# Optimization experiments

Hardware: AMD Instinct MI355X
Metric: run time of the kernel (lower is better)

Reference implementation:

```python
import jax, jax.numpy as jnp
import numpy as np

N_NODES = 100000
N_EDGES = 1600000
IN_DIM, HID_DIM, OUT_DIM = 128, 128, 64


def _sage_conv(x, src, dst, W_l, W_r, b, num_nodes):
    # messages: gather source-node features, mean-aggregate at destination
    msgs = x[src]                                            # [E, D]
    agg = jax.ops.segment_sum(msgs, dst, num_segments=num_nodes)   # [N, D]
    deg = jax.ops.segment_sum(jnp.ones((src.shape[0],), x.dtype), dst,
                              num_segments=num_nodes)        # [N]
    mean = jnp.where(deg[:, None] > 0, agg / jnp.maximum(deg, 1.0)[:, None], 0.0)
    # PyG SAGEConv: lin_l(aggr) + lin_r(root); bias lives in lin_l
    return mean @ W_l + b + x @ W_r


def setup_inputs() -> dict:
    key = jax.random.key(0)
    ks = jax.random.split(key, 8)
    x = jax.random.normal(ks[0], (N_NODES, IN_DIM), dtype=jnp.float32)
    edge_index = jax.random.randint(ks[1], (2, N_EDGES), 0, N_NODES, dtype=jnp.int64)
    s1 = 1.0 / np.sqrt(IN_DIM)
    s2 = 1.0 / np.sqrt(HID_DIM)
    return {
        "x": x,
        "edge_index": edge_index,
        "W1_l": jax.random.normal(ks[2], (IN_DIM, HID_DIM), jnp.float32) * s1,
        "W1_r": jax.random.normal(ks[3], (IN_DIM, HID_DIM), jnp.float32) * s1,
        "b1": jnp.zeros((HID_DIM,), jnp.float32),
        "W2_l": jax.random.normal(ks[4], (HID_DIM, OUT_DIM), jnp.float32) * s2,
        "W2_r": jax.random.normal(ks[5], (HID_DIM, OUT_DIM), jnp.float32) * s2,
        "b2": jnp.zeros((OUT_DIM,), jnp.float32),
    }


def reference(x, edge_index, W1_l, W1_r, b1, W2_l, W2_r, b2):
    src, dst = edge_index[0], edge_index[1]  # source_to_target flow
    h = _sage_conv(x, src, dst, W1_l, W1_r, b1, N_NODES)
    h = jax.nn.relu(h)
    # dropout is identity in eval mode
    h = _sage_conv(h, src, dst, W2_l, W2_r, b2, N_NODES)
    return h
```

## Files before the change

kernel.cpp:

```cpp
#include <hip/hip_runtime.h>

#define N_NODES 100000
#define N_EDGES 1600000
#define IN_DIM 128
#define HID_DIM 128
#define OUT_DIM 64

#define BKT_SHIFT 8
#define NPB 256
#define NBKT ((N_NODES + NPB - 1) / NPB)
#define BKT_CAP 5120
#define BIN_CHUNK 4096

#define CC_CSR NBKT
#define CC_CONV (N_NODES / 4)
#define CC_WT 192

typedef __attribute__((ext_vector_type(8))) short short8;
typedef __attribute__((ext_vector_type(4))) float f32x4;
typedef __attribute__((ext_vector_type(2))) short s16x2;

__device__ __forceinline__ float bf2f(unsigned short h) {
    unsigned int u = ((unsigned int)h) << 16;
    return __builtin_bit_cast(float, u);
}
__device__ __forceinline__ unsigned short f2bf(float f) {
    unsigned int u = __builtin_bit_cast(unsigned int, f);
    u += 0x7FFFu + ((u >> 16) & 1u);
    return (unsigned short)(u >> 16);
}

#define XSCALE 21.166666f
#define XINV   0.047244094f
#define ZQ     10.583333f
#define ZINV   0.094488189f

__device__ __forceinline__ void acc_i8x4(unsigned v, s16x2& L, s16x2& H) {
    s16x2 sv = __builtin_bit_cast(s16x2, v);
    H += sv >> 8;
    L += (s16x2)(sv << 8) >> 8;
}
__device__ __forceinline__ s16x2 shfl_down_pk(s16x2 a, int off) {
    return __builtin_bit_cast(s16x2, __shfl_down(__builtin_bit_cast(int, a), off, 64));
}

__device__ __forceinline__ int wswz(int m, int k, int KW) {
    return (m * KW + k) ^ ((m & 7) << 3);
}

__global__ __launch_bounds__(256) void bin_kernel(
        const int* __restrict__ src, const int* __restrict__ dst,
        int* __restrict__ cursor, unsigned* __restrict__ binned) {
    __shared__ int cnt[NBKT];
    __shared__ int sbase[NBKT];
    const int b = blockIdx.x, t = threadIdx.x;
    for (int i = t; i < NBKT; i += 256) cnt[i] = 0;
    __syncthreads();
    const int e0 = b * BIN_CHUNK;
    unsigned val[16];
    int bkt[16], rank[16];
    #pragma unroll
    for (int k = 0; k < 16; ++k) {
        int e = e0 + k * 256 + t;
        if (e < N_EDGES) {
            int d = dst[e];
            bkt[k] = d >> BKT_SHIFT;
            val[k] = (unsigned)src[e] | ((unsigned)(d & (NPB - 1)) << 17);
            rank[k] = atomicAdd(&cnt[bkt[k]], 1);
        } else {
            bkt[k] = -1;
        }
    }
    __syncthreads();
    for (int i = t; i < NBKT; i += 256)
        sbase[i] = cnt[i] ? atomicAdd(&cursor[i], cnt[i]) : 0;
    __syncthreads();
    #pragma unroll
    for (int k = 0; k < 16; ++k)
        if (bkt[k] >= 0)
            binned[(size_t)bkt[k] * BKT_CAP + sbase[bkt[k]] + rank[k]] = val[k];
}

__global__ __launch_bounds__(256) void csr_conv_kernel(
        const unsigned* __restrict__ binned, const int* __restrict__ cursor,
        int* __restrict__ offsets, int* __restrict__ csr_src,
        const float* __restrict__ x, unsigned short* __restrict__ xh,
        unsigned char* __restrict__ xq,
        const float* __restrict__ W1l, const float* __restrict__ W1r,
        const float* __restrict__ W2l, const float* __restrict__ W2r,
        unsigned short* __restrict__ WT1, unsigned short* __restrict__ WT2T) {
    int b = blockIdx.x;
    const int t = threadIdx.x;

    if (b < CC_CSR) {
        __shared__ int deg[NPB];
        __shared__ int cur[NPB];
        __shared__ int wsums[4];
        __shared__ int sbase_sh;
        const int lane = t & 63, wid = t >> 6;

        int ps = 0;
        for (int i = t; i < b; i += 256) ps += cursor[i];
        #pragma unroll
        for (int off = 32; off; off >>= 1) ps += __shfl_down(ps, off, 64);
        if (lane == 0) wsums[wid] = ps;
        deg[t] = 0;
        __syncthreads();
        if (t == 0) sbase_sh = wsums[0] + wsums[1] + wsums[2] + wsums[3];
        __syncthreads();
        const int base = sbase_sh;
        const int n0 = b << BKT_SHIFT;
        const int cnt = cursor[b];
        const unsigned* __restrict__ ebase = binned + (size_t)b * BKT_CAP;

        for (int i = t; i < cnt; i += 256)
            atomicAdd(&deg[ebase[i] >> 17], 1);
        __syncthreads();

        int d = deg[t];
        int s = d;
        #pragma unroll
        for (int off = 1; off < 64; off <<= 1) {
            int u = __shfl_up(s, off, 64);
            if (lane >= off) s += u;
        }
        if (lane == 63) wsums[wid] = s;
        __syncthreads();
        int add = 0;
        for (int w = 0; w < wid; ++w) add += wsums[w];
        const int excl = s + add - d;
        cur[t] = excl;
        const int n = n0 + t;
        if (n <= N_NODES) offsets[n] = base + excl;
        __syncthreads();

        for (int i = t; i < cnt; i += 256) {
            unsigned v = ebase[i];
            int pos = atomicAdd(&cur[v >> 17], 1);
            csr_src[base + pos] = (int)(v & 0x1FFFFu);
        }
        return;
    }

    b -= CC_CSR;
    if (b < CC_CONV) {
        const int w = t >> 6, lane = t & 63;
        const int row = b * 4 + w;
        float2 v = *(const float2*)(x + (size_t)row * 128 + lane * 2);
        unsigned pk = (unsigned)f2bf(v.x) | ((unsigned)f2bf(v.y) << 16);
        *(unsigned*)(xh + (size_t)row * 128 + lane * 2) = pk;
        int q0 = (int)__float2int_rn(fminf(fmaxf(v.x * XSCALE, -127.f), 127.f));
        int q1 = (int)__float2int_rn(fminf(fmaxf(v.y * XSCALE, -127.f), 127.f));
        *(unsigned short*)(xq + (size_t)row * 128 + lane * 2) =
            (unsigned short)((q0 & 0xFF) | ((q1 & 0xFF) << 8));
        return;
    }

    int i = (b - CC_CONV) * 256 + t;
    if (i < 128 * 256) {
        int m = i >> 8, k = i & 255;
        float v = (k < 128) ? W1l[(size_t)k * 128 + m] : W1r[(size_t)(k - 128) * 128 + m];
        WT1[wswz(m, k, 256)] = f2bf(v);
        return;
    }
    i -= 128 * 256;
    if (i < 128 * 128) {
        int j = i >> 7, k = i & 127;
        float v = (j < 64) ? W2l[(size_t)k * 64 + j] : W2r[(size_t)k * 64 + (j - 64)];
        WT2T[wswz(j, k, 128)] = f2bf(v);
    }
}

__global__ __launch_bounds__(256) void agg1_int8(
        const unsigned char* __restrict__ xq, const int* __restrict__ offsets,
        const int* __restrict__ csr_src, unsigned short* __restrict__ mh) {
    const int node = blockIdx.x * 4 + (threadIdx.x >> 6);
    const int lane = threadIdx.x & 63;
    const int q = lane >> 3, dp = lane & 7;
    const int beg = offsets[node], end = offsets[node + 1];
    const int deg = end - beg;

    if (deg == 0) {
        if (q == 0) {
            uint4 z = {0u, 0u, 0u, 0u};
            ((uint4*)(mh + (size_t)node * 128 + dp * 16))[0] = z;
            ((uint4*)(mh + (size_t)node * 128 + dp * 16))[1] = z;
        }
        return;
    }

    s16x2 aL[4], aH[4];
    #pragma unroll
    for (int i = 0; i < 4; ++i) { aL[i] = (s16x2)0; aH[i] = (s16x2)0; }

    const int idxv = csr_src[beg + (lane < deg ? lane : 0)];
    const int nb = deg < 64 ? deg : 64;

    #pragma unroll 2
    for (int e0 = 0; e0 < nb; e0 += 8) {
        int ei = e0 + q;
        int s = __shfl(idxv, ei < 63 ? ei : 63, 64);
        if (ei < nb) {
            uint4 v = *(const uint4*)(xq + (size_t)s * 128 + dp * 16);
            acc_i8x4(v.x, aL[0], aH[0]);
            acc_i8x4(v.y, aL[1], aH[1]);
            acc_i8x4(v.z, aL[2], aH[2]);
            acc_i8x4(v.w, aL[3], aH[3]);
        }
    }
    if (deg > 64) {
        for (int j = beg + 64; j < end; j += 8) {
            if (j + q < end) {
                int s = csr_src[j + q];
                uint4 v = *(const uint4*)(xq + (size_t)s * 128 + dp * 16);
                acc_i8x4(v.x, aL[0], aH[0]);
                acc_i8x4(v.y, aL[1], aH[1]);
                acc_i8x4(v.z, aL[2], aH[2]);
                acc_i8x4(v.w, aL[3], aH[3]);
            }
        }
    }
    #pragma unroll
    for (int i = 0; i < 4; ++i) {
        #pragma unroll
        for (int off = 8; off < 64; off <<= 1) {
            aL[i] += shfl_down_pk(aL[i], off);
            aH[i] += shfl_down_pk(aH[i], off);
        }
    }
    if (q == 0) {
        const float inv = XINV / (float)deg;
        unsigned w[8];
        #pragma unroll
        for (int d = 0; d < 4; ++d) {
            w[2 * d]     = (unsigned)f2bf((float)aL[d].x * inv)
                         | ((unsigned)f2bf((float)aH[d].x * inv) << 16);
            w[2 * d + 1] = (unsigned)f2bf((float)aL[d].y * inv)
                         | ((unsigned)f2bf((float)aH[d].y * inv) << 16);
        }
        uint4* o = (uint4*)(mh + (size_t)node * 128 + dp * 16);
        o[0] = make_uint4(w[0], w[1], w[2], w[3]);
        o[1] = make_uint4(w[4], w[5], w[6], w[7]);
    }
}

__global__ __launch_bounds__(256) void gemm1_kernel(
        const unsigned short* __restrict__ mh, const unsigned short* __restrict__ xh,
        const unsigned short* __restrict__ WT1, const float* __restrict__ b1,
        unsigned short* __restrict__ hh) {
    __shared__ unsigned short Ws[128 * 256];
    const int t = threadIdx.x;
    {
        const uint4* s = (const uint4*)WT1;
        uint4* d = (uint4*)Ws;
        #pragma unroll
        for (int r = 0; r < 16; ++r) d[t + r * 256] = s[t + r * 256];
    }
    const int wave = t >> 6;
    const int lane = t & 63;
    const int rowbase = blockIdx.x * 128 + wave * 32;
    const int lrow = lane & 15;
    const int kq = (lane >> 4) * 8;
    const int rsw = (lrow & 7) << 3;

    f32x4 acc[2][8];
    #pragma unroll
    for (int rt = 0; rt < 2; ++rt)
        #pragma unroll
        for (int ct = 0; ct < 8; ++ct) acc[rt][ct] = (f32x4)0.f;

    int r0 = rowbase + lrow;      if (r0 > N_NODES - 1) r0 = N_NODES - 1;
    int r1 = rowbase + 16 + lrow; if (r1 > N_NODES - 1) r1 = N_NODES - 1;

    __syncthreads();

    #pragma unroll
    for (int half = 0; half < 2; ++half) {
        const unsigned short* __restrict__ A = half ? xh : mh;
        #pragma unroll
        for (int kc = 0; kc < 4; ++kc) {
            const int kofs = kc * 32 + kq;
            short8 a0 = *(const short8*)(A + (size_t)r0 * 128 + kofs);
            short8 a1 = *(const short8*)(A + (size_t)r1 * 128 + kofs);
            #pragma unroll
            for (int ct = 0; ct < 8; ++ct) {
                short8 bb = *(const short8*)&Ws[(((ct * 16 + lrow) << 8)
                                                 + (half << 7) + kofs) ^ rsw];
                acc[0][ct] = __builtin_amdgcn_mfma_f32_16x16x32_bf16(a0, bb, acc[0][ct], 0, 0, 0);
                acc[1][ct] = __builtin_amdgcn_mfma_f32_16x16x32_bf16(a1, bb, acc[1][ct], 0, 0, 0);
            }
        }
    }

    const int colq = lane & 15;
    const int rowq = (lane >> 4) * 4;
    #pragma unroll
    for (int ct = 0; ct < 8; ++ct) {
        const int col = ct * 16 + colq;
        const float bc = b1[col];
        #pragma unroll
        for (int rt = 0; rt < 2; ++rt) {
            #pragma unroll
            for (int i = 0; i < 4; ++i) {
                const int row = rowbase + rt * 16 + rowq + i;
                if (row < N_NODES)
                    hh[(size_t)row * 128 + col] = f2bf(fmaxf(acc[rt][ct][i] + bc, 0.f));
            }
        }
    }
}

__global__ __launch_bounds__(256) void gemm2_kernel(
        const unsigned short* __restrict__ hh, const unsigned short* __restrict__ WT2T,
        const float* __restrict__ b2, unsigned char* __restrict__ zq,
        unsigned short* __restrict__ pout) {
    __shared__ unsigned short Ws[128 * 128];
    const int t = threadIdx.x;
    {
        const uint4* s = (const uint4*)WT2T;
        uint4* d = (uint4*)Ws;
        #pragma unroll
        for (int r = 0; r < 8; ++r) d[t + r * 256] = s[t + r * 256];
    }
    const int wave = t >> 6;
    const int lane = t & 63;
    const int rowbase = blockIdx.x * 128 + wave * 32;
    const int lrow = lane & 15;
    const int kq = (lane >> 4) * 8;
    const int rsw = (lrow & 7) << 3;

    f32x4 acc[2][8];
    #pragma unroll
    for (int rt = 0; rt < 2; ++rt)
        #pragma unroll
        for (int ct = 0; ct < 8; ++ct) acc[rt][ct] = (f32x4)0.f;

    int r0 = rowbase + lrow;      if (r0 > N_NODES - 1) r0 = N_NODES - 1;
    int r1 = rowbase + 16 + lrow; if (r1 > N_NODES - 1) r1 = N_NODES - 1;

    __syncthreads();

    #pragma unroll
    for (int kc = 0; kc < 4; ++kc) {
        const int kofs = kc * 32 + kq;
        short8 a0 = *(const short8*)(hh + (size_t)r0 * 128 + kofs);
        short8 a1 = *(const short8*)(hh + (size_t)r1 * 128 + kofs);
        #pragma unroll
        for (int ct = 0; ct < 8; ++ct) {
            short8 bb = *(const short8*)&Ws[(((ct * 16 + lrow) << 7) + kofs) ^ rsw];
            acc[0][ct] = __builtin_amdgcn_mfma_f32_16x16x32_bf16(a0, bb, acc[0][ct], 0, 0, 0);
            acc[1][ct] = __builtin_amdgcn_mfma_f32_16x16x32_bf16(a1, bb, acc[1][ct], 0, 0, 0);
        }
    }

    const int colq = lane & 15;
    const int rowq = (lane >> 4) * 4;

    #pragma unroll
    for (int rt = 0; rt < 2; ++rt) {
        #pragma unroll
        for (int i = 0; i < 4; ++i) {
            const int row = rowbase + rt * 16 + rowq + i;
            if (row < N_NODES) {
                unsigned char* zr = zq + (size_t)row * 64 + colq;
                #pragma unroll
                for (int ct = 0; ct < 4; ++ct) {
                    float v = fminf(fmaxf(acc[rt][ct][i] * ZQ, -127.f), 127.f);
                    zr[ct * 16] = (unsigned char)(signed char)__float2int_rn(v);
                }
            }
        }
    }
    #pragma unroll
    for (int ct = 4; ct < 8; ++ct) {
        const int col = ct * 16 + colq;
        const float bc = b2[col - 64];
        #pragma unroll
        for (int rt = 0; rt < 2; ++rt) {
            #pragma unroll
            for (int i = 0; i < 4; ++i) {
                const int row = rowbase + rt * 16 + rowq + i;
                if (row < N_NODES)
                    pout[(size_t)row * 64 + (col - 64)] = f2bf(acc[rt][ct][i] + bc);
            }
        }
    }
}

__global__ __launch_bounds__(256) void agg2_out_kernel(
        const unsigned char* __restrict__ zq, const unsigned short* __restrict__ pout,
        const int* __restrict__ offsets, const int* __restrict__ csr_src,
        float* __restrict__ out) {
    const int node = blockIdx.x * 4 + (threadIdx.x >> 6);
    const int lane = threadIdx.x & 63;
    const int q = lane >> 2, dp = lane & 3;
    const int beg = offsets[node], end = offsets[node + 1];
    const int deg = end - beg;

    s16x2 aL[4], aH[4];
    #pragma unroll
    for (int i = 0; i < 4; ++i) { aL[i] = (s16x2)0; aH[i] = (s16x2)0; }

    if (deg > 0) {
        const int idxv = csr_src[beg + (lane < deg ? lane : 0)];
        const int nb = deg < 64 ? deg : 64;
        #pragma unroll 4
        for (int e0 = 0; e0 < nb; e0 += 16) {
            int ei = e0 + q;
            int s = __shfl(idxv, ei < 63 ? ei : 63, 64);
            if (ei < nb) {
                uint4 v = *(const uint4*)(zq + (size_t)s * 64 + dp * 16);
                acc_i8x4(v.x, aL[0], aH[0]);
                acc_i8x4(v.y, aL[1], aH[1]);
                acc_i8x4(v.z, aL[2], aH[2]);
                acc_i8x4(v.w, aL[3], aH[3]);
            }
        }
        if (deg > 64) {
            for (int j = beg + 64; j < end; j += 16) {
                if (j + q < end) {
                    int s = csr_src[j + q];
                    uint4 v = *(const uint4*)(zq + (size_t)s * 64 + dp * 16);
                    acc_i8x4(v.x, aL[0], aH[0]);
                    acc_i8x4(v.y, aL[1], aH[1]);
                    acc_i8x4(v.z, aL[2], aH[2]);
                    acc_i8x4(v.w, aL[3], aH[3]);
                }
            }
        }
        #pragma unroll
        for (int i = 0; i < 4; ++i) {
            #pragma unroll
            for (int off = 4; off < 64; off <<= 1) {
                aL[i] += shfl_down_pk(aL[i], off);
                aH[i] += shfl_down_pk(aH[i], off);
            }
        }
    }
    if (q == 0) {
        const float inv = (deg > 0) ? ZINV / (float)deg : 0.0f;
        const unsigned short* pp = pout + (size_t)node * 64 + dp * 16;
        float* oo = out + (size_t)node * 64 + dp * 16;
        #pragma unroll
        for (int d = 0; d < 4; ++d) {
            ushort4 p = *(const ushort4*)(pp + d * 4);
            float4 o;
            o.x = (float)aL[d].x * inv + bf2f(p.x);
            o.y = (float)aH[d].x * inv + bf2f(p.y);
            o.z = (float)aL[d].y * inv + bf2f(p.z);
            o.w = (float)aH[d].y * inv + bf2f(p.w);
            *(float4*)(oo + d * 4) = o;
        }
    }
}


extern "C" void kernel_launch(void* const* d_in, const int* in_sizes, int n_in,
                              void* d_out, int out_size, void* d_ws, size_t ws_size,
                              hipStream_t stream) {
    const float* x   = (const float*)d_in[0];
    const int*   ei  = (const int*)d_in[1];
    const float* W1l = (const float*)d_in[2];
    const float* W1r = (const float*)d_in[3];
    const float* b1  = (const float*)d_in[4];
    const float* W2l = (const float*)d_in[5];
    const float* W2r = (const float*)d_in[6];
    const float* b2  = (const float*)d_in[7];
    float* out = (float*)d_out;

    const int* src = ei;
    const int* dst = ei + N_EDGES;

    char* ws = (char*)d_ws;
    int* cursor   = (int*)ws;
    int* offsets  = cursor + 512;
    int* csr_src  = offsets + N_NODES + 16;
    unsigned char*  xq  = (unsigned char*)(csr_src + N_EDGES + 64);
    unsigned short* xh  = (unsigned short*)(xq + (size_t)N_NODES * 128);
    unsigned short* mh  = xh + (size_t)N_NODES * 128;
    unsigned short* hh  = mh + (size_t)N_NODES * 128;
    unsigned char*  zq  = (unsigned char*)(hh + (size_t)N_NODES * 128);
    unsigned short* pout = (unsigned short*)(zq + (size_t)N_NODES * 64);
    unsigned short* WT1  = pout + (size_t)N_NODES * 64;
    unsigned short* WT2T = WT1 + 128 * 256;
    unsigned* binned = (unsigned*)mh;

    hipMemsetAsync(cursor, 0, NBKT * sizeof(int), stream);

    bin_kernel<<<(N_EDGES + BIN_CHUNK - 1) / BIN_CHUNK, 256, 0, stream>>>(
        src, dst, cursor, binned);

    csr_conv_kernel<<<CC_CSR + CC_CONV + CC_WT, 256, 0, stream>>>(
        binned, cursor, offsets, csr_src, x, xh, xq,
        W1l, W1r, W2l, W2r, WT1, WT2T);

    agg1_int8<<<N_NODES / 4, 256, 0, stream>>>(xq, offsets, csr_src, mh);
    gemm1_kernel<<<(N_NODES + 127) / 128, 256, 0, stream>>>(mh, xh, WT1, b1, hh);

    gemm2_kernel<<<(N_NODES + 127) / 128, 256, 0, stream>>>(hh, WT2T, b2, zq, pout);
    agg2_out_kernel<<<N_NODES / 4, 256, 0, stream>>>(zq, pout, offsets, csr_src, out);
}
```

Before: 202.1 us.

## Map eight nodes per wave in aggregation kernels to remove cross-lane reductions

Both aggregation kernels now assign one node to each 8-lane group, so a wave handles eight nodes instead of one. Each lane owns a fixed slice of the feature row and loops over that node's whole neighbor list. Neighbor indices are loaded eight at a time and broadcast with shuffles. This removes the shuffle-down reductions, the separate path for degrees above 64, and the idle lanes on low-degree nodes. In exchange, lanes in a wave can diverge when their nodes have different degrees, and agg2 now issues 8-byte loads per lane instead of 16-byte loads.

```diff
diff --git a/kernel.cpp b/kernel.cpp
--- a/kernel.cpp
+++ b/kernel.cpp
@@ -39,9 +39,6 @@
     s16x2 sv = __builtin_bit_cast(s16x2, v);
     H += sv >> 8;
     L += (s16x2)(sv << 8) >> 8;
-}
-__device__ __forceinline__ s16x2 shfl_down_pk(s16x2 a, int off) {
-    return __builtin_bit_cast(s16x2, __shfl_down(__builtin_bit_cast(int, a), off, 64));
 }
 
 __device__ __forceinline__ int wswz(int m, int k, int KW) {
@@ -174,44 +171,24 @@
 __global__ __launch_bounds__(256) void agg1_int8(
         const unsigned char* __restrict__ xq, const int* __restrict__ offsets,
         const int* __restrict__ csr_src, unsigned short* __restrict__ mh) {
-    const int node = blockIdx.x * 4 + (threadIdx.x >> 6);
+    const int wv = threadIdx.x >> 6;
     const int lane = threadIdx.x & 63;
-    const int q = lane >> 3, dp = lane & 7;
-    const int beg = offsets[node], end = offsets[node + 1];
-    const int deg = end - beg;
-
-    if (deg == 0) {
-        if (q == 0) {
-            uint4 z = {0u, 0u, 0u, 0u};
-            ((uint4*)(mh + (size_t)node * 128 + dp * 16))[0] = z;
-            ((uint4*)(mh + (size_t)node * 128 + dp * 16))[1] = z;
-        }
-        return;
-    }
+    const int slot = lane >> 3, dp = lane & 7;
+    const int node = (blockIdx.x * 4 + wv) * 8 + slot;
+    const int beg = offsets[node];
+    const int deg = offsets[node + 1] - beg;
 
     s16x2 aL[4], aH[4];
     #pragma unroll
     for (int i = 0; i < 4; ++i) { aL[i] = (s16x2)0; aH[i] = (s16x2)0; }
 
-    const int idxv = csr_src[beg + (lane < deg ? lane : 0)];
-    const int nb = deg < 64 ? deg : 64;
-
-    #pragma unroll 2
-    for (int e0 = 0; e0 < nb; e0 += 8) {
-        int ei = e0 + q;
-        int s = __shfl(idxv, ei < 63 ? ei : 63, 64);
-        if (ei < nb) {
-            uint4 v = *(const uint4*)(xq + (size_t)s * 128 + dp * 16);
-            acc_i8x4(v.x, aL[0], aH[0]);
-            acc_i8x4(v.y, aL[1], aH[1]);
-            acc_i8x4(v.z, aL[2], aH[2]);
-            acc_i8x4(v.w, aL[3], aH[3]);
-        }
-    }
-    if (deg > 64) {
-        for (int j = beg + 64; j < end; j += 8) {
-            if (j + q < end) {
-                int s = csr_src[j + q];
+    for (int c = 0; c < deg; c += 8) {
+        int my = beg + c + dp;
+        int idx8 = csr_src[my < beg + deg ? my : beg];
+        #pragma unroll
+        for (int jj = 0; jj < 8; ++jj) {
+            if (c + jj < deg) {
+                int s = __shfl(idx8, slot * 8 + jj, 64);
                 uint4 v = *(const uint4*)(xq + (size_t)s * 128 + dp * 16);
                 acc_i8x4(v.x, aL[0], aH[0]);
                 acc_i8x4(v.y, aL[1], aH[1]);
@@ -220,28 +197,19 @@
             }
         }
     }
-    #pragma unroll
-    for (int i = 0; i < 4; ++i) {
-        #pragma unroll
-        for (int off = 8; off < 64; off <<= 1) {
-            aL[i] += shfl_down_pk(aL[i], off);
-            aH[i] += shfl_down_pk(aH[i], off);
-        }
-    }
-    if (q == 0) {
-        const float inv = XINV / (float)deg;
-        unsigned w[8];
-        #pragma unroll
-        for (int d = 0; d < 4; ++d) {
-            w[2 * d]     = (unsigned)f2bf((float)aL[d].x * inv)
-                         | ((unsigned)f2bf((float)aH[d].x * inv) << 16);
-            w[2 * d + 1] = (unsigned)f2bf((float)aL[d].y * inv)
-                         | ((unsigned)f2bf((float)aH[d].y * inv) << 16);
-        }
-        uint4* o = (uint4*)(mh + (size_t)node * 128 + dp * 16);
-        o[0] = make_uint4(w[0], w[1], w[2], w[3]);
-        o[1] = make_uint4(w[4], w[5], w[6], w[7]);
-    }
+
+    const float inv = (deg > 0) ? XINV / (float)deg : 0.0f;
+    unsigned w[8];
+    #pragma unroll
+    for (int d = 0; d < 4; ++d) {
+        w[2 * d]     = (unsigned)f2bf((float)aL[d].x * inv)
+                     | ((unsigned)f2bf((float)aH[d].x * inv) << 16);
+        w[2 * d + 1] = (unsigned)f2bf((float)aL[d].y * inv)
+                     | ((unsigned)f2bf((float)aH[d].y * inv) << 16);
+    }
+    uint4* o = (uint4*)(mh + (size_t)node * 128 + dp * 16);
+    o[0] = make_uint4(w[0], w[1], w[2], w[3]);
+    o[1] = make_uint4(w[4], w[5], w[6], w[7]);
 }
 
 __global__ __launch_bounds__(256) void gemm1_kernel(
@@ -391,66 +359,43 @@
         const unsigned char* __restrict__ zq, const unsigned short* __restrict__ pout,
         const int* __restrict__ offsets, const int* __restrict__ csr_src,
         float* __restrict__ out) {
-    const int node = blockIdx.x * 4 + (threadIdx.x >> 6);
+    const int wv = threadIdx.x >> 6;
     const int lane = threadIdx.x & 63;
-    const int q = lane >> 2, dp = lane & 3;
-    const int beg = offsets[node], end = offsets[node + 1];
-    const int deg = end - beg;
-
-    s16x2 aL[4], aH[4];
-    #pragma unroll
-    for (int i = 0; i < 4; ++i) { aL[i] = (s16x2)0; aH[i] = (s16x2)0; }
-
-    if (deg > 0) {
-        const int idxv = csr_src[beg + (lane < deg ? lane : 0)];
-        const int nb = deg < 64 ? deg : 64;
-        #pragma unroll 4
-        for (int e0 = 0; e0 < nb; e0 += 16) {
-            int ei = e0 + q;
-            int s = __shfl(idxv, ei < 63 ? ei : 63, 64);
-            if (ei < nb) {
-                uint4 v = *(const uint4*)(zq + (size_t)s * 64 + dp * 16);
+    const int slot = lane >> 3, dp = lane & 7;
+    const int node = (blockIdx.x * 4 + wv) * 8 + slot;
+    const int beg = offsets[node];
+    const int deg = offsets[node + 1] - beg;
+
+    s16x2 aL[2], aH[2];
+    #pragma unroll
+    for (int i = 0; i < 2; ++i) { aL[i] = (s16x2)0; aH[i] = (s16x2)0; }
+
+    for (int c = 0; c < deg; c += 8) {
+        int my = beg + c + dp;
+        int idx8 = csr_src[my < beg + deg ? my : beg];
+        #pragma unroll
+        for (int jj = 0; jj < 8; ++jj) {
+            if (c + jj < deg) {
+                int s = __shfl(idx8, slot * 8 + jj, 64);
+                uint2 v = *(const uint2*)(zq + (size_t)s * 64 + dp * 8);
                 acc_i8x4(v.x, aL[0], aH[0]);
                 acc_i8x4(v.y, aL[1], aH[1]);
-                acc_i8x4(v.z, aL[2], aH[2]);
-                acc_i8x4(v.w, aL[3], aH[3]);
-            }
-        }
-        if (deg > 64) {
-            for (int j = beg + 64; j < end; j += 16) {
-                if (j + q < end) {
-                    int s = csr_src[j + q];
-                    uint4 v = *(const uint4*)(zq + (size_t)s * 64 + dp * 16);
-                    acc_i8x4(v.x, aL[0], aH[0]);
-                    acc_i8x4(v.y, aL[1], aH[1]);
-                    acc_i8x4(v.z, aL[2], aH[2]);
-                    acc_i8x4(v.w, aL[3], aH[3]);
-                }
-            }
-        }
-        #pragma unroll
-        for (int i = 0; i < 4; ++i) {
-            #pragma unroll
-            for (int off = 4; off < 64; off <<= 1) {
-                aL[i] += shfl_down_pk(aL[i], off);
-                aH[i] += shfl_down_pk(aH[i], off);
-            }
-        }
-    }
-    if (q == 0) {
-        const float inv = (deg > 0) ? ZINV / (float)deg : 0.0f;
-        const unsigned short* pp = pout + (size_t)node * 64 + dp * 16;
-        float* oo = out + (size_t)node * 64 + dp * 16;
-        #pragma unroll
-        for (int d = 0; d < 4; ++d) {
-            ushort4 p = *(const ushort4*)(pp + d * 4);
-            float4 o;
-            o.x = (float)aL[d].x * inv + bf2f(p.x);
-            o.y = (float)aH[d].x * inv + bf2f(p.y);
-            o.z = (float)aL[d].y * inv + bf2f(p.z);
-            o.w = (float)aH[d].y * inv + bf2f(p.w);
-            *(float4*)(oo + d * 4) = o;
-        }
+            }
+        }
+    }
+
+    const float inv = (deg > 0) ? ZINV / (float)deg : 0.0f;
+    const unsigned short* pp = pout + (size_t)node * 64 + dp * 8;
+    float* oo = out + (size_t)node * 64 + dp * 8;
+    #pragma unroll
+    for (int d = 0; d < 2; ++d) {
+        ushort4 p = *(const ushort4*)(pp + d * 4);
+        float4 o;
+        o.x = (float)aL[d].x * inv + bf2f(p.x);
+        o.y = (float)aH[d].x * inv + bf2f(p.y);
+        o.z = (float)aL[d].y * inv + bf2f(p.z);
+        o.w = (float)aH[d].y * inv + bf2f(p.w);
+        *(float4*)(oo + d * 4) = o;
     }
 }
 
@@ -494,9 +439,9 @@
         binned, cursor, offsets, csr_src, x, xh, xq,
         W1l, W1r, W2l, W2r, WT1, WT2T);
 
-    agg1_int8<<<N_NODES / 4, 256, 0, stream>>>(xq, offsets, csr_src, mh);
+    agg1_int8<<<N_NODES / 32, 256, 0, stream>>>(xq, offsets, csr_src, mh);
     gemm1_kernel<<<(N_NODES + 127) / 128, 256, 0, stream>>>(mh, xh, WT1, b1, hh);
 
     gemm2_kernel<<<(N_NODES + 127) / 128, 256, 0, stream>>>(hh, WT2T, b2, zq, pout);
-    agg2_out_kernel<<<N_NODES / 4, 256, 0, stream>>>(zq, pout, offsets, csr_src, out);
-}
+    agg2_out_kernel<<<N_NODES / 32, 256, 0, stream>>>(zq, pout, offsets, csr_src, out);
+}
```

Measured after the change: 193.5 us. 1.04x faster.
